# Kernel tuning notes

Hardware: AMD Instinct MI355X
Metric: run time of the kernel (lower is better)

Reference implementation:

```python
import jax, jax.numpy as jnp
import numpy as np

D, H, B, T = 256, 512, 16, 512

def setup_inputs() -> dict:
    key = jax.random.key(0)
    ks = jax.random.split(key, 4)
    x = jax.random.normal(ks[0], (B, T, D), dtype=jnp.float32)
    W_w = jax.random.normal(ks[1], (4 * H, D), dtype=jnp.float32) / np.sqrt(D)
    U_w = jax.random.normal(ks[2], (4 * H, H), dtype=jnp.float32) / np.sqrt(H)
    V_w = jax.random.normal(ks[3], (H, D * H), dtype=jnp.float32) / np.sqrt(D * H)
    return {
        "x": x,
        "W_w": W_w, "W_b": jnp.zeros((4 * H,), jnp.float32),
        "U_w": U_w, "U_b": jnp.zeros((4 * H,), jnp.float32),
        "V_w": V_w, "V_b": jnp.zeros((H,), jnp.float32),
    }

def reference(x, W_w, W_b, U_w, U_b, V_w, V_b):
    Bz, Tz, Dz = x.shape
    Hz = U_w.shape[1]
    # Precompute input projections for all timesteps in one big GEMM: (B,T,4H)
    wx_all = jnp.einsum('btd,gd->btg', x, W_w) + W_b

    def step(carry, inputs):
        h, c = carry
        xt, wx = inputs  # xt: (B,D), wx: (B,4H)
        gates = wx + h @ U_w.T + U_b
        i, f, o, g = jnp.split(gates, 4, axis=-1)
        i, f, o, g = jax.nn.sigmoid(i), jax.nn.sigmoid(f), jax.nn.sigmoid(o), jnp.tanh(g)
        # outer product x_t (B,D) x h (B,H) -> (B, D*H), row-major like torch reshape
        mult = (xt[:, :, None] * h[:, None, :]).reshape(Bz, Dz * Hz)
        m = jnp.tanh(mult @ V_w.T + V_b)
        c = f * c + i * g + 0.1 * m
        h = o * jnp.tanh(c)
        return (h, c), h

    h0 = jnp.zeros((Bz, Hz), x.dtype)
    c0 = jnp.zeros((Bz, Hz), x.dtype)
    (hT, cT), outs = jax.lax.scan(
        step, (h0, c0), (jnp.swapaxes(x, 0, 1), jnp.swapaxes(wx_all, 0, 1)))
    outs = jnp.swapaxes(outs, 0, 1)  # (B,T,H)
    return outs, (hT, cT)
```

## Files before the change

kernel.cpp:

```cpp
#include <hip/hip_runtime.h>
#include <cstdint>
#include <cstddef>

#define Dk 256
#define Hk 512
#define Bk 16
#define Tk 512
#define Gk 2048
#define NVk 262144

typedef __bf16 bf16;
typedef __bf16 bf16x8 __attribute__((ext_vector_type(8)));
typedef float  f32x4  __attribute__((ext_vector_type(4)));
typedef const __attribute__((address_space(1))) void* gvp;
typedef __attribute__((address_space(3))) void* lvp;

__device__ __forceinline__ float bflo(unsigned u) {
  u <<= 16; return __builtin_bit_cast(float, u);
}
__device__ __forceinline__ float bfhi(unsigned u) {
  u &= 0xffff0000u; return __builtin_bit_cast(float, u);
}

__global__ __launch_bounds__(256) void cvt_f32_bf16(const float* __restrict__ in,
                                                    bf16* __restrict__ out, int n8) {
  int i = blockIdx.x * 256 + threadIdx.x;
  if (i >= n8) return;
  const float4* p = reinterpret_cast<const float4*>(in) + (size_t)i * 2;
  float4 a = p[0], b = p[1];
  bf16x8 v;
  v[0] = (bf16)a.x; v[1] = (bf16)a.y; v[2] = (bf16)a.z; v[3] = (bf16)a.w;
  v[4] = (bf16)b.x; v[5] = (bf16)b.y; v[6] = (bf16)b.z; v[7] = (bf16)b.w;
  *reinterpret_cast<bf16x8*>(out + (size_t)i * 8) = v;
}

__global__ __launch_bounds__(256) void pack_V(const float* __restrict__ Vw,
                                              bf16* __restrict__ V2p) {
  int n = blockIdx.x * 256 + threadIdx.x;
  int j = n >> 9, hp = n & 511;
  const float* src = Vw + (size_t)j * 131072 + hp;
  for (int kb = 0; kb < 32; ++kb) {
    bf16x8 v;
#pragma unroll
    for (int r = 0; r < 8; ++r) v[r] = (bf16)src[(size_t)(kb * 8 + r) * 512];
    *reinterpret_cast<bf16x8*>(V2p + ((size_t)kb * NVk + n) * 8) = v;
  }
}

__global__ __launch_bounds__(256) void pack_W(const float* __restrict__ Ww,
                                              bf16* __restrict__ Wp) {
  int g = blockIdx.x * 256 + threadIdx.x;
  const float* src = Ww + (size_t)g * 256;
  for (int kb = 0; kb < 32; ++kb) {
    bf16x8 v;
#pragma unroll
    for (int r = 0; r < 8; ++r) v[r] = (bf16)src[kb * 8 + r];
    *reinterpret_cast<bf16x8*>(Wp + ((size_t)kb * Gk + g) * 8) = v;
  }
}

__global__ __launch_bounds__(256) void pack_x(const float* __restrict__ x,
                                              bf16* __restrict__ xp) {
  int row = blockIdx.x * 256 + threadIdx.x;
  const float* src = x + (size_t)row * 256;
  for (int kb = 0; kb < 32; ++kb) {
    bf16x8 v;
#pragma unroll
    for (int r = 0; r < 8; ++r) v[r] = (bf16)src[kb * 8 + r];
    *reinterpret_cast<bf16x8*>(xp + ((size_t)kb * 8192 + row) * 8) = v;
  }
}

__global__ __launch_bounds__(256) void init_state(bf16* __restrict__ hbuf,
                                                  float* __restrict__ cws) {
  int i = blockIdx.x * 256 + threadIdx.x;
  if (i < 16384) hbuf[i] = (bf16)0.f;
  if (i < 8192)  cws[i]  = 0.f;
}

template <bool BF16_OUT>
__global__ __launch_bounds__(256) void gemm128(const bf16* __restrict__ Ap,
                                               const bf16* __restrict__ Bp,
                                               float* __restrict__ outF,
                                               bf16* __restrict__ outB,
                                               const float* __restrict__ bias,
                                               const float* __restrict__ bias2,
                                               int N, int Mtot,
                                               int t0, int tcMask, int tcShift) {
  __shared__ uint4 a_sm[512];
  __shared__ uint4 b_sm[512];
  int tid = threadIdx.x;
  int lane = tid & 63, w = tid >> 6;
  int quad = lane >> 4, l15 = lane & 15;
  int wm = w >> 1, wn = w & 1;
  int m0 = blockIdx.x * 128, n0 = blockIdx.y * 128;

  f32x4 acc[4][4];
#pragma unroll
  for (int i = 0; i < 4; ++i)
#pragma unroll
    for (int j = 0; j < 4; ++j) acc[i][j] = (f32x4){0.f, 0.f, 0.f, 0.f};

  int gm0 = m0 + lane, gm1 = m0 + 64 + lane;
  int xr0 = ((gm0 >> tcShift) << 9) + t0 + (gm0 & tcMask);
  int xr1 = ((gm1 >> tcShift) << 9) + t0 + (gm1 & tcMask);
  const uint4* gA = reinterpret_cast<const uint4*>(Ap);
  const uint4* gB = reinterpret_cast<const uint4*>(Bp);

  const bf16x8* aptr = reinterpret_cast<const bf16x8*>(a_sm);
  const bf16x8* bptr = reinterpret_cast<const bf16x8*>(b_sm);

  for (int kk = 0; kk < 8; ++kk) {
    size_t kbg = (size_t)(kk * 4 + w);
    __builtin_amdgcn_global_load_lds((gvp)(gA + kbg * Mtot + xr0),
                                     (lvp)(&a_sm[w * 128]), 16, 0, 0);
    __builtin_amdgcn_global_load_lds((gvp)(gA + kbg * Mtot + xr1),
                                     (lvp)(&a_sm[w * 128 + 64]), 16, 0, 0);
    __builtin_amdgcn_global_load_lds((gvp)(gB + kbg * N + n0 + lane),
                                     (lvp)(&b_sm[w * 128]), 16, 0, 0);
    __builtin_amdgcn_global_load_lds((gvp)(gB + kbg * N + n0 + 64 + lane),
                                     (lvp)(&b_sm[w * 128 + 64]), 16, 0, 0);
    __syncthreads();
    bf16x8 af[4], bfr[4];
#pragma unroll
    for (int i = 0; i < 4; ++i) af[i]  = aptr[quad * 128 + wm * 64 + i * 16 + l15];
#pragma unroll
    for (int j = 0; j < 4; ++j) bfr[j] = bptr[quad * 128 + wn * 64 + j * 16 + l15];
#pragma unroll
    for (int i = 0; i < 4; ++i)
#pragma unroll
      for (int j = 0; j < 4; ++j)
        acc[i][j] = __builtin_amdgcn_mfma_f32_16x16x32_bf16(af[i], bfr[j], acc[i][j], 0, 0, 0);
    __syncthreads();
  }

#pragma unroll
  for (int i = 0; i < 4; ++i) {
    int row = m0 + wm * 64 + i * 16 + quad * 4;
#pragma unroll
    for (int j = 0; j < 4; ++j) {
      int col = n0 + wn * 64 + j * 16 + l15;
      f32x4 v = acc[i][j];
      if (BF16_OUT) {
#pragma unroll
        for (int r = 0; r < 4; ++r)
          outB[(size_t)(row + r) * N + col] = (bf16)v[r];
      } else {
        float bv = bias[col] + bias2[col];
#pragma unroll
        for (int r = 0; r < 4; ++r)
          outF[(size_t)(row + r) * N + col] = v[r] + bv;
      }
    }
  }
}

__global__ __launch_bounds__(256) void scan_step3(
    const bf16* __restrict__ A,
    int trel, int Tc,
    const bf16* __restrict__ Ubf,
    const float* __restrict__ wx,
    const float* __restrict__ Vb,
    const bf16* __restrict__ hprev,
    bf16* __restrict__ hnext,
    float* __restrict__ cst,
    float* __restrict__ out, int t) {
  __shared__ bf16 U_s[4 * Hk];
  __shared__ float gate_s[64];
  __shared__ float m_s[16];
  int tid = threadIdx.x;
  int j = blockIdx.x;
  int b = tid >> 4, sm = tid & 15;

  const bf16* Ar = A + ((size_t)b * Tc + trel) * NVk + (size_t)j * Hk;
  uint4 av[4];
#pragma unroll
  for (int i = 0; i < 4; ++i)
    av[i] = *reinterpret_cast<const uint4*>(Ar + i * 128 + sm * 8);

  uint4 hv[4];
#pragma unroll
  for (int i = 0; i < 4; ++i)
    hv[i] = *reinterpret_cast<const uint4*>(hprev + b * Hk + i * 128 + sm * 8);

  {
    int r = tid >> 6, e = (tid & 63) * 8;
    *reinterpret_cast<uint4*>(U_s + r * Hk + e) =
        *reinterpret_cast<const uint4*>(Ubf + ((size_t)r * Hk + j) * Hk + e);
  }
  __syncthreads();

  float hf[4][8];
#pragma unroll
  for (int i = 0; i < 4; ++i) {
    unsigned ux = hv[i].x, uy = hv[i].y, uz = hv[i].z, uw = hv[i].w;
    hf[i][0] = bflo(ux); hf[i][1] = bfhi(ux);
    hf[i][2] = bflo(uy); hf[i][3] = bfhi(uy);
    hf[i][4] = bflo(uz); hf[i][5] = bfhi(uz);
    hf[i][6] = bflo(uw); hf[i][7] = bfhi(uw);
  }

  float accs[5] = {0.f, 0.f, 0.f, 0.f, 0.f};
  const uint4* Uq = reinterpret_cast<const uint4*>(U_s);
#pragma unroll
  for (int i = 0; i < 4; ++i) {
#pragma unroll
    for (int q = 0; q < 4; ++q) {
      uint4 u = Uq[q * 64 + i * 16 + sm];
      accs[q] += bflo(u.x) * hf[i][0] + bfhi(u.x) * hf[i][1]
               + bflo(u.y) * hf[i][2] + bfhi(u.y) * hf[i][3]
               + bflo(u.z) * hf[i][4] + bfhi(u.z) * hf[i][5]
               + bflo(u.w) * hf[i][6] + bfhi(u.w) * hf[i][7];
    }
    uint4 a = av[i];
    accs[4] += bflo(a.x) * hf[i][0] + bfhi(a.x) * hf[i][1]
             + bflo(a.y) * hf[i][2] + bfhi(a.y) * hf[i][3]
             + bflo(a.z) * hf[i][4] + bfhi(a.z) * hf[i][5]
             + bflo(a.w) * hf[i][6] + bfhi(a.w) * hf[i][7];
  }
#pragma unroll
  for (int d = 1; d < 16; d <<= 1) {
#pragma unroll
    for (int k = 0; k < 5; ++k) accs[k] += __shfl_xor(accs[k], d);
  }
  if (sm == 0) {
    const float* wxr = wx + ((size_t)b * Tk + t) * Gk + j;
#pragma unroll
    for (int q = 0; q < 4; ++q) gate_s[q * 16 + b] = accs[q] + wxr[q * Hk];
    m_s[b] = accs[4];
  }
  __syncthreads();

  if (tid < 16) {
    int bb = tid;
    float gi = gate_s[bb], gf = gate_s[16 + bb];
    float go = gate_s[32 + bb], gg = gate_s[48 + bb];
    float iv = 1.f / (1.f + __expf(-gi));
    float fv = 1.f / (1.f + __expf(-gf));
    float ov = 1.f / (1.f + __expf(-go));
    float gv = tanhf(gg);
    float mv = tanhf(m_s[bb] + Vb[j]);
    int idx = bb * Hk + j;
    float c = fv * cst[idx] + iv * gv + 0.1f * mv;
    cst[idx] = c;
    float h = ov * tanhf(c);
    hnext[idx] = (bf16)h;
    out[((size_t)bb * Tk + t) * Hk + j] = h;
    if (t == Tk - 1) {
      out[(size_t)Bk * Tk * Hk + idx] = h;
      out[(size_t)Bk * Tk * Hk + Bk * Hk + idx] = c;
    }
  }
}

extern "C" void kernel_launch(void* const* d_in, const int* in_sizes, int n_in,
                              void* d_out, int out_size, void* d_ws, size_t ws_size,
                              hipStream_t stream) {
  const float* x  = (const float*)d_in[0];
  const float* Ww = (const float*)d_in[1];
  const float* Wb = (const float*)d_in[2];
  const float* Uw = (const float*)d_in[3];
  const float* Ub = (const float*)d_in[4];
  const float* Vw = (const float*)d_in[5];
  const float* Vb = (const float*)d_in[6];
  float* out = (float*)d_out;

  char* ws = (char*)d_ws;
  size_t off = 0;
  auto alloc = [&](size_t bytes) -> void* {
    void* p = ws + off;
    off = (off + bytes + 255) & ~(size_t)255;
    return p;
  };
  bf16*  xp   = (bf16*)alloc((size_t)Bk * Tk * Dk * 2);
  bf16*  V2p  = (bf16*)alloc((size_t)32 * NVk * 8 * 2);
  bf16*  Wp   = (bf16*)alloc((size_t)32 * Gk * 8 * 2);
  bf16*  Ubf  = (bf16*)alloc((size_t)Gk * Hk * 2);
  float* wx   = (float*)alloc((size_t)Bk * Tk * Gk * 4);
  bf16*  hbuf = (bf16*)alloc((size_t)16384 * 2);
  float* cws  = (float*)alloc((size_t)8192 * 4);
  size_t fixedBytes = off;

  int Tc = 512;
  while (Tc > 8 && fixedBytes + (size_t)Bk * Tc * Hk * Hk * 2 > ws_size) Tc >>= 1;
  bf16* A_ws = (bf16*)alloc((size_t)Bk * Tc * Hk * Hk * 2);
  int tcShift = 31 - __builtin_clz((unsigned)Tc);

  pack_x<<<32, 256, 0, stream>>>(x, xp);
  cvt_f32_bf16<<<512, 256, 0, stream>>>(Uw, Ubf, 131072);
  pack_V<<<1024, 256, 0, stream>>>(Vw, V2p);
  pack_W<<<8, 256, 0, stream>>>(Ww, Wp);
  init_state<<<64, 256, 0, stream>>>(hbuf, cws);

  gemm128<false><<<dim3(64, 16), 256, 0, stream>>>(xp, Wp, wx, nullptr, Wb, Ub,
                                                   Gk, 8192, 0, 511, 9);

  for (int c0 = 0; c0 < Tk; c0 += Tc) {
    gemm128<true><<<dim3(Bk * Tc / 128, NVk / 128), 256, 0, stream>>>(
        xp, V2p, nullptr, A_ws, nullptr, nullptr, NVk, 8192, c0, Tc - 1, tcShift);
    for (int t = c0; t < c0 + Tc; ++t) {
      scan_step3<<<512, 256, 0, stream>>>(
          A_ws, t - c0, Tc, Ubf, wx, Vb,
          hbuf + (t & 1) * 8192, hbuf + ((t + 1) & 1) * 8192,
          cws, out, t);
    }
  }
}
```

Measured before the change: 5.947 ms.

## Replace per-timestep scan launches with persistent cooperative kernel and grid barrier

Swaps the 512 per-timestep scan_step3 launches for one cooperative persistent kernel that loops over timesteps and synchronises all 512 blocks through a hierarchical atomic grid barrier. The U slice and the cell state stay on chip in shared memory and registers across steps, and the next step's A row is prefetched into registers while the current step computes. This is meant to remove launch overhead and per-step reloads of U and c. It depends on cooperative launch succeeding and falls back to the old per-step kernels otherwise, and the grid barrier adds its own per-step sync latency.

```diff
diff --git a/kernel.cpp b/kernel.cpp
--- a/kernel.cpp
+++ b/kernel.cpp
@@ -8,6 +8,7 @@
 #define Tk 512
 #define Gk 2048
 #define NVk 262144
+#define NBLK 512
 
 typedef __bf16 bf16;
 typedef __bf16 bf16x8 __attribute__((ext_vector_type(8)));
@@ -72,10 +73,12 @@
 }
 
 __global__ __launch_bounds__(256) void init_state(bf16* __restrict__ hbuf,
-                                                  float* __restrict__ cws) {
+                                                  float* __restrict__ cws,
+                                                  int* __restrict__ bar) {
   int i = blockIdx.x * 256 + threadIdx.x;
   if (i < 16384) hbuf[i] = (bf16)0.f;
   if (i < 8192)  cws[i]  = 0.f;
+  if (i < 256)   bar[i]  = 0;
 }
 
 template <bool BF16_OUT>
@@ -156,15 +159,11 @@
 }
 
 __global__ __launch_bounds__(256) void scan_step3(
-    const bf16* __restrict__ A,
-    int trel, int Tc,
-    const bf16* __restrict__ Ubf,
-    const float* __restrict__ wx,
+    const bf16* __restrict__ A, int trel, int Tc,
+    const bf16* __restrict__ Ubf, const float* __restrict__ wx,
     const float* __restrict__ Vb,
-    const bf16* __restrict__ hprev,
-    bf16* __restrict__ hnext,
-    float* __restrict__ cst,
-    float* __restrict__ out, int t) {
+    const bf16* __restrict__ hprev, bf16* __restrict__ hnext,
+    float* __restrict__ cst, float* __restrict__ out, int t) {
   __shared__ bf16 U_s[4 * Hk];
   __shared__ float gate_s[64];
   __shared__ float m_s[16];
@@ -253,6 +252,144 @@
   }
 }
 
+__device__ __forceinline__ void gbar512(int* bar) {
+  __syncthreads();
+  if (threadIdx.x == 0) {
+    int g = __hip_atomic_load(bar + 192, __ATOMIC_RELAXED, __HIP_MEMORY_SCOPE_AGENT);
+    int grp = (int)blockIdx.x >> 6;
+    int a = __hip_atomic_fetch_add(bar + grp * 16, 1, __ATOMIC_ACQ_REL,
+                                   __HIP_MEMORY_SCOPE_AGENT);
+    if (a == 63) {
+      __hip_atomic_store(bar + grp * 16, 0, __ATOMIC_RELAXED, __HIP_MEMORY_SCOPE_AGENT);
+      int b2 = __hip_atomic_fetch_add(bar + 160, 1, __ATOMIC_ACQ_REL,
+                                      __HIP_MEMORY_SCOPE_AGENT);
+      if (b2 == 7) {
+        __hip_atomic_store(bar + 160, 0, __ATOMIC_RELAXED, __HIP_MEMORY_SCOPE_AGENT);
+        __hip_atomic_store(bar + 192, g + 1, __ATOMIC_RELEASE, __HIP_MEMORY_SCOPE_AGENT);
+      }
+    }
+    while (__hip_atomic_load(bar + 192, __ATOMIC_RELAXED, __HIP_MEMORY_SCOPE_AGENT) == g)
+      __builtin_amdgcn_s_sleep(1);
+    (void)__hip_atomic_load(bar + 192, __ATOMIC_ACQUIRE, __HIP_MEMORY_SCOPE_AGENT);
+  }
+  __syncthreads();
+}
+
+__global__ __launch_bounds__(256, 2) void scan_persist(
+    const bf16* __restrict__ A, int Tc, int c0,
+    const bf16* __restrict__ Ubf, const float* __restrict__ wx,
+    const float* __restrict__ Vb, bf16* __restrict__ hbuf,
+    float* __restrict__ cst, float* __restrict__ out, int* __restrict__ bar) {
+  __shared__ bf16 U_s[4 * Hk];
+  __shared__ float gate_s[64];
+  __shared__ float m_s[16];
+  int tid = threadIdx.x;
+  int j = blockIdx.x;
+  int b = tid >> 4, sm = tid & 15;
+
+  {
+    int r = tid >> 6, e = (tid & 63) * 8;
+    *reinterpret_cast<uint4*>(U_s + r * Hk + e) =
+        *reinterpret_cast<const uint4*>(Ubf + ((size_t)r * Hk + j) * Hk + e);
+  }
+  float c_reg = (tid < 16) ? cst[tid * Hk + j] : 0.f;
+  float vb = Vb[j];
+  __syncthreads();
+
+  const uint4* Aq = reinterpret_cast<const uint4*>(A);
+  const uint4* Uq = reinterpret_cast<const uint4*>(U_s);
+  size_t abase = (size_t)(b * Tc) * 32768 + (size_t)j * 64 + sm;
+
+  uint4 avA[4], avB[4];
+#pragma unroll
+  for (int i = 0; i < 4; ++i) avA[i] = Aq[abase + i * 16];
+
+  for (int trel = 0; trel < Tc; ++trel) {
+    int t = c0 + trel;
+    const bf16* hprev = hbuf + (t & 1) * 8192;
+    bf16* hnext = hbuf + ((t + 1) & 1) * 8192;
+
+    uint4 hv[4];
+#pragma unroll
+    for (int i = 0; i < 4; ++i)
+      hv[i] = *reinterpret_cast<const uint4*>(hprev + b * Hk + i * 128 + sm * 8);
+
+    float wxq[4] = {0.f, 0.f, 0.f, 0.f};
+    if (sm == 0) {
+      const float* wxr = wx + ((size_t)b * Tk + t) * Gk + j;
+#pragma unroll
+      for (int q = 0; q < 4; ++q) wxq[q] = wxr[q * Hk];
+    }
+
+    float accs[5] = {0.f, 0.f, 0.f, 0.f, 0.f};
+#pragma unroll
+    for (int i = 0; i < 4; ++i) {
+      float hf[8];
+      unsigned ux = hv[i].x, uy = hv[i].y, uz = hv[i].z, uw = hv[i].w;
+      hf[0] = bflo(ux); hf[1] = bfhi(ux);
+      hf[2] = bflo(uy); hf[3] = bfhi(uy);
+      hf[4] = bflo(uz); hf[5] = bfhi(uz);
+      hf[6] = bflo(uw); hf[7] = bfhi(uw);
+#pragma unroll
+      for (int q = 0; q < 4; ++q) {
+        uint4 u = Uq[q * 64 + i * 16 + sm];
+        accs[q] += bflo(u.x) * hf[0] + bfhi(u.x) * hf[1]
+                 + bflo(u.y) * hf[2] + bfhi(u.y) * hf[3]
+                 + bflo(u.z) * hf[4] + bfhi(u.z) * hf[5]
+                 + bflo(u.w) * hf[6] + bfhi(u.w) * hf[7];
+      }
+      uint4 a = avA[i];
+      accs[4] += bflo(a.x) * hf[0] + bfhi(a.x) * hf[1]
+               + bflo(a.y) * hf[2] + bfhi(a.y) * hf[3]
+               + bflo(a.z) * hf[4] + bfhi(a.z) * hf[5]
+               + bflo(a.w) * hf[6] + bfhi(a.w) * hf[7];
+    }
+
+    if (trel + 1 < Tc) {
+      size_t nb = abase + (size_t)(trel + 1) * 32768;
+#pragma unroll
+      for (int i = 0; i < 4; ++i) avB[i] = Aq[nb + i * 16];
+    }
+
+#pragma unroll
+    for (int d = 1; d < 16; d <<= 1) {
+#pragma unroll
+      for (int k = 0; k < 5; ++k) accs[k] += __shfl_xor(accs[k], d);
+    }
+    if (sm == 0) {
+#pragma unroll
+      for (int q = 0; q < 4; ++q) gate_s[q * 16 + b] = accs[q] + wxq[q];
+      m_s[b] = accs[4];
+    }
+    __syncthreads();
+
+    if (tid < 16) {
+      float gi = gate_s[tid], gf = gate_s[16 + tid];
+      float go = gate_s[32 + tid], gg = gate_s[48 + tid];
+      float iv = 1.f / (1.f + __expf(-gi));
+      float fv = 1.f / (1.f + __expf(-gf));
+      float ov = 1.f / (1.f + __expf(-go));
+      float gv = tanhf(gg);
+      float mv = tanhf(m_s[tid] + vb);
+      float c = fv * c_reg + iv * gv + 0.1f * mv;
+      c_reg = c;
+      float h = ov * tanhf(c);
+      hnext[tid * Hk + j] = (bf16)h;
+      out[((size_t)tid * Tk + t) * Hk + j] = h;
+      if (t == Tk - 1) {
+        out[(size_t)Bk * Tk * Hk + tid * Hk + j] = h;
+        out[(size_t)Bk * Tk * Hk + Bk * Hk + tid * Hk + j] = c;
+      }
+    }
+
+    gbar512(bar);
+
+#pragma unroll
+    for (int i = 0; i < 4; ++i) avA[i] = avB[i];
+  }
+  if (tid < 16) cst[tid * Hk + j] = c_reg;
+}
+
 extern "C" void kernel_launch(void* const* d_in, const int* in_sizes, int n_in,
                               void* d_out, int out_size, void* d_ws, size_t ws_size,
                               hipStream_t stream) {
@@ -279,6 +416,7 @@
   float* wx   = (float*)alloc((size_t)Bk * Tk * Gk * 4);
   bf16*  hbuf = (bf16*)alloc((size_t)16384 * 2);
   float* cws  = (float*)alloc((size_t)8192 * 4);
+  int*   bar  = (int*)alloc(256 * sizeof(int));
   size_t fixedBytes = off;
 
   int Tc = 512;
@@ -290,7 +428,7 @@
   cvt_f32_bf16<<<512, 256, 0, stream>>>(Uw, Ubf, 131072);
   pack_V<<<1024, 256, 0, stream>>>(Vw, V2p);
   pack_W<<<8, 256, 0, stream>>>(Ww, Wp);
-  init_state<<<64, 256, 0, stream>>>(hbuf, cws);
+  init_state<<<64, 256, 0, stream>>>(hbuf, cws, bar);
 
   gemm128<false><<<dim3(64, 16), 256, 0, stream>>>(xp, Wp, wx, nullptr, Wb, Ub,
                                                    Gk, 8192, 0, 511, 9);
@@ -298,11 +436,19 @@
   for (int c0 = 0; c0 < Tk; c0 += Tc) {
     gemm128<true><<<dim3(Bk * Tc / 128, NVk / 128), 256, 0, stream>>>(
         xp, V2p, nullptr, A_ws, nullptr, nullptr, NVk, 8192, c0, Tc - 1, tcShift);
-    for (int t = c0; t < c0 + Tc; ++t) {
-      scan_step3<<<512, 256, 0, stream>>>(
-          A_ws, t - c0, Tc, Ubf, wx, Vb,
-          hbuf + (t & 1) * 8192, hbuf + ((t + 1) & 1) * 8192,
-          cws, out, t);
-    }
-  }
-}
+
+    int TcV = Tc, c0V = c0;
+    void* args[] = {(void*)&A_ws, (void*)&TcV, (void*)&c0V, (void*)&Ubf,
+                    (void*)&wx, (void*)&Vb, (void*)&hbuf, (void*)&cws,
+                    (void*)&out, (void*)&bar};
+    hipError_t e = hipLaunchCooperativeKernel((const void*)scan_persist,
+                                              dim3(NBLK), dim3(256), args, 0, stream);
+    if (e != hipSuccess) {
+      for (int t = c0; t < c0 + Tc; ++t)
+        scan_step3<<<512, 256, 0, stream>>>(
+            A_ws, t - c0, Tc, Ubf, wx, Vb,
+            hbuf + (t & 1) * 8192, hbuf + ((t + 1) & 1) * 8192,
+            cws, out, t);
+    }
+  }
+}
```

Result: slower. 14.49 ms (+143.7%).
